# Optimization experiments

Measured on AMD Instinct MI355X. Metric: run time of the kernel, lower is better.

The kernel has to match this reference:

```python
import jax, jax.numpy as jnp
import numpy as np

B, T, D = 256, 336, 128
H = 1024
N_LABEL, LABEL_CLASS = 24, 1
FORGET_BIAS = 1.0  # TF BasicLSTMCell default


def setup_inputs() -> dict:
    key = jax.random.key(0)
    ks = jax.random.split(key, 8)
    s1 = 1.0 / np.sqrt(D + H)
    s2 = 1.0 / np.sqrt(2 * H)
    sd = 1.0 / np.sqrt(H)
    return {
        "features": jax.random.normal(ks[0], (B, T, D), jnp.float32),
        "labels": jax.random.normal(ks[1], (B, N_LABEL, LABEL_CLASS), jnp.float32),
        "W1": jax.random.normal(ks[2], (D + H, 4 * H), jnp.float32) * s1,
        "b1": jnp.zeros((4 * H,), jnp.float32),
        "W2": jax.random.normal(ks[3], (2 * H, 4 * H), jnp.float32) * s2,
        "b2": jnp.zeros((4 * H,), jnp.float32),
        "Wd": jax.random.normal(ks[4], (H, N_LABEL * LABEL_CLASS), jnp.float32) * sd,
        "bd": jnp.zeros((N_LABEL * LABEL_CLASS,), jnp.float32),
    }


def _lstm_cell(c, h, x, W, b):
    # TF BasicLSTMCell: gates = [x, h] @ W + b, split into i, j, f, o
    z = jnp.concatenate([x, h], axis=-1) @ W + b
    i, j, f, o = jnp.split(z, 4, axis=-1)
    new_c = c * jax.nn.sigmoid(f + FORGET_BIAS) + jax.nn.sigmoid(i) * jnp.tanh(j)
    new_h = jnp.tanh(new_c) * jax.nn.sigmoid(o)
    return new_c, new_h


def reference(features, labels, W1, b1, W2, b2, Wd, bd):
    batch = features.shape[0]
    zeros = jnp.zeros((batch, H), features.dtype)
    init = (zeros, zeros, zeros, zeros)  # c1, h1, c2, h2

    def step(carry, x_t):
        c1, h1, c2, h2 = carry
        c1, h1 = _lstm_cell(c1, h1, x_t, W1, b1)
        c2, h2 = _lstm_cell(c2, h2, h1, W2, b2)
        return (c1, h1, c2, h2), None

    xs = jnp.swapaxes(features, 0, 1)  # [T, B, D]
    (c1, h1, c2, h2), _ = jax.lax.scan(step, init, xs)
    # dense head on last-timestep output of top layer
    pred = (h2 @ Wd + bd).reshape(batch, N_LABEL, LABEL_CLASS)
    loss = jnp.mean(jnp.square(pred - labels))
    return loss
```

## Files before the change

### kernel.cpp

```cpp
#include <hip/hip_runtime.h>

#define TT 336
#define BB 256
#define DD 128
#define HH 1024
#define TD 43008
#define BBHH 262144

#define SSU0 20480u
#define SSU1 32768u
#define LBU1 5242880u

typedef __attribute__((ext_vector_type(8))) short short8;
typedef __attribute__((ext_vector_type(8))) unsigned short ushort8;
typedef __attribute__((ext_vector_type(4))) unsigned short ushort4v;
typedef __attribute__((ext_vector_type(4))) float floatx4;

#define OFF_ZPAD 0u
#define OFF_C1   4096u
#define OFF_C2   1052672u
#define OFF_H1   2101248u
#define OFF_H2   3149824u
#define OFF_B1P  4198400u
#define OFF_B2P  4214784u
#define OFF_X    4231168u
#define OFF_BP   26251264u

static __device__ __forceinline__ unsigned short f2bf(float f) {
  unsigned int x = __float_as_uint(f);
  x += 0x7fffu + ((x >> 16) & 1u);
  return (unsigned short)(x >> 16);
}
static __device__ __forceinline__ float bf2f(unsigned short u) {
  return __uint_as_float(((unsigned int)u) << 16);
}
static __device__ __forceinline__ float sigm(float x) {
  return 1.f / (1.f + __expf(-x));
}
static __device__ __forceinline__ float tanh_fast(float x) {
  float ax = fabsf(x);
  float e = __expf(-2.f * ax);
  float t = (1.f - e) / (1.f + e);
  return x < 0.f ? -t : t;
}

#define GLOAD_LDS16(gsrc, ldst)                                              \
  __builtin_amdgcn_global_load_lds(                                          \
      (const __attribute__((address_space(1))) void*)(gsrc),                 \
      (__attribute__((address_space(3))) void*)(ldst), 16, 0, 0)

__global__ __launch_bounds__(256) void init_zero(float* out, uint4* span, long n16) {
  long i = (long)blockIdx.x * 256 + threadIdx.x;
  if (i < n16) span[i] = make_uint4(0u, 0u, 0u, 0u);
  if (i == 0) out[0] = 0.f;
}

__global__ __launch_bounds__(256) void feat2bf(const float* __restrict__ in,
                                               unsigned short* __restrict__ out, long nq) {
  long Q = (long)blockIdx.x * 256 + threadIdx.x;
  if (Q >= nq) return;
  int b = (int)(Q / 5376);
  long outQ = (Q & ~7L) | ((Q ^ (long)b) & 7);
  const floatx4* pp = (const floatx4*)(in + Q * 8);
  floatx4 a = pp[0], c = pp[1];
  ushort8 v;
  #pragma unroll
  for (int q = 0; q < 4; ++q) { v[q] = f2bf(a[q]); v[4 + q] = f2bf(c[q]); }
  *(ushort8*)(out + outQ * 8) = v;
}

__global__ __launch_bounds__(256) void bpack(const float* __restrict__ W1,
                                             const float* __restrict__ W2,
                                             unsigned short* __restrict__ out) {
  __shared__ unsigned short tile[64][72];
  int bid = blockIdx.x, t = threadIdx.x;
  int L, tk, tn;
  if (bid < 1280) { L = 0; tk = bid % 20; tn = bid / 20; }
  else            { L = 1; tk = (bid - 1280) % 32; tn = (bid - 1280) / 32; }
  const float* W = L ? W2 : W1;
  int KG = L ? 512 : 320;
  int k0 = tk * 64, n0p = tn * 64;
  int g = k0 / KG;
  int ksg0 = (k0 - g * KG) >> 5;
  int ntile = n0p >> 7, wn = (n0p >> 6) & 1;
  unsigned int SSu = L ? SSU1 : SSU0;
  unsigned int base = (L ? LBU1 : 0u) + ntile * 8u * SSu + (g * 2 + wn) * SSu;

  #pragma unroll
  for (int i = 0; i < 16; ++i) {
    int idx = i * 256 + t;
    int kk = idx >> 6, nn = idx & 63;
    int np = n0p + nn;
    int norig = ((np & 3) << 10) + (np >> 2);
    float v = 0.f;
    if (!(L == 0 && k0 + kk >= 1152)) v = W[(size_t)(k0 + kk) * 4096 + norig];
    tile[kk][nn] = f2bf(v);
  }
  __syncthreads();
  int t64 = t & 63;
  #pragma unroll
  for (int pass = 0; pass < 2; ++pass) {
    int f = (t >> 6) + pass * 4;
    int ksl = f >> 2, ni = f & 3;
    ushort8 v;
    #pragma unroll
    for (int j = 0; j < 8; ++j)
      v[j] = tile[ksl * 32 + ((t64 >> 4) << 3) + j][ni * 16 + (t64 & 15)];
    *(ushort8*)(out + base + (unsigned)((ksg0 + ksl) * 4 + ni) * 512u + t64 * 8) = v;
  }
}

__global__ __launch_bounds__(256) void bias_perm(const float* __restrict__ b1,
                                                 const float* __restrict__ b2,
                                                 float* __restrict__ b1p,
                                                 float* __restrict__ b2p) {
  int idx = blockIdx.x * 256 + threadIdx.x;
  const float* src = (idx < 4096) ? b1 : b2;
  float* dst = (idx < 4096) ? b1p : b2p;
  int n = idx & 4095;
  dst[n] = src[(n & 3) * 1024 + (n >> 2)];
}

__global__ __launch_bounds__(512, 2) void gemm_cell(
    const unsigned short* __restrict__ Xbf,
    unsigned short* __restrict__ h1bufs, unsigned short* __restrict__ h2bufs,
    const unsigned short* __restrict__ Bpack,
    const float* __restrict__ b1p, const float* __restrict__ b2p,
    float* __restrict__ c1, float* __restrict__ c2,
    const unsigned short* __restrict__ zpad,
    int p, int do1, int do2) {
  __shared__ __align__(16) unsigned short Abuf[4][2][64 * 64];
  __shared__ __align__(16) float zt0[64 * 132];
  __shared__ __align__(16) float zt1[64 * 132];

  int bid = blockIdx.x;
  int layer = bid >> 7;
  if (layer == 0 ? !do1 : !do2) return;
  int lid = bid & 127;
  int ntile = (lid & 7) | (((lid >> 5) & 3) << 3);
  int mtile = (lid >> 3) & 3;
  int m0 = mtile * 64;
  int u0 = ntile * 32;

  const unsigned short* hp1 = h1bufs + (size_t)(p & 1) * BBHH;
  const unsigned short* hp2 = h2bufs + (size_t)(p & 1) * BBHH;
  const int KG = layer ? 512 : 320;
  const int NIT = KG >> 6;

  int tid = threadIdx.x;
  int g = tid >> 7;
  int wn = (tid >> 6) & 1;
  int lane = tid & 63;
  int kgbase = g * KG;

  unsigned int SSu = layer ? SSU1 : SSU0;
  const unsigned short* bwave =
      Bpack + (layer ? LBU1 : 0u) + ntile * 8u * SSu + (unsigned)(g * 2 + wn) * SSu;

  auto stageA = [&](int buf, int it) {
    int kb = kgbase + (it << 6);
    unsigned short* dst0 = &Abuf[g][buf][0];
    #pragma unroll
    for (int c = 0; c < 4; ++c) {
      int rowbase = c * 16 + wn * 8;
      int rg = m0 + rowbase + (lane >> 3);
      int kq = lane & 7;
      const unsigned short* src;
      if (layer == 0) {
        if (kb < DD)        src = Xbf + (size_t)rg * TD + p * DD + kb + kq * 8;
        else if (kb < 1152) src = hp1 + (size_t)rg * HH + (kb - DD) + kq * 8;
        else                src = zpad + lane * 8;
      } else {
        if (kb < HH) src = hp1 + (size_t)rg * HH + kb + kq * 8;
        else         src = hp2 + (size_t)rg * HH + (kb - HH) + kq * 8;
      }
      GLOAD_LDS16(src, dst0 + rowbase * 64);
    }
  };
  auto loadB = [&](ushort8 (&dst)[2][4], int it) {
    #pragma unroll
    for (int ksl = 0; ksl < 2; ++ksl)
      #pragma unroll
      for (int ni = 0; ni < 4; ++ni)
        dst[ksl][ni] =
            *(const ushort8*)(bwave + (unsigned)((it * 2 + ksl) * 4 + ni) * 512u + lane * 8);
  };

  floatx4 acc[4][4];
  #pragma unroll
  for (int i = 0; i < 4; ++i)
    #pragma unroll
    for (int j = 0; j < 4; ++j) acc[i][j] = (floatx4){0.f, 0.f, 0.f, 0.f};

  ushort8 bc[2][4], bn[2][4];
  stageA(0, 0);
  loadB(bc, 0);

  for (int it = 0; it < NIT; ++it) {
    int buf = it & 1;
    __syncthreads();
    if (it + 1 < NIT) { stageA(buf ^ 1, it + 1); loadB(bn, it + 1); }
    const unsigned short* Ab = &Abuf[g][buf][0];
    #pragma unroll
    for (int ksl = 0; ksl < 2; ++ksl) {
      int qb = ksl * 4 + (lane >> 4);
      short8 af[4];
      #pragma unroll
      for (int mi = 0; mi < 4; ++mi) {
        int ml = mi * 16 + (lane & 15);
        af[mi] = *(const short8*)&Ab[ml * 64 + ((qb ^ (ml & 7)) << 3)];
      }
      #pragma unroll
      for (int mi = 0; mi < 4; ++mi)
        #pragma unroll
        for (int ni = 0; ni < 4; ++ni)
          acc[mi][ni] = __builtin_amdgcn_mfma_f32_16x16x32_bf16(
              af[mi], (short8)bc[ksl][ni], acc[mi][ni], 0, 0, 0);
    }
    #pragma unroll
    for (int ksl = 0; ksl < 2; ++ksl)
      #pragma unroll
      for (int ni = 0; ni < 4; ++ni) bc[ksl][ni] = bn[ksl][ni];
  }

  float* ztw = (g & 1) ? zt1 : zt0;
  if (g < 2) {
    #pragma unroll
    for (int mi = 0; mi < 4; ++mi)
      #pragma unroll
      for (int ni = 0; ni < 4; ++ni)
        #pragma unroll
        for (int rr = 0; rr < 4; ++rr) {
          int row = mi * 16 + (lane >> 4) * 4 + rr;
          int col = wn * 64 + ni * 16 + (lane & 15);
          ztw[row * 132 + col] = acc[mi][ni][rr];
        }
  }
  __syncthreads();
  if (g >= 2) {
    #pragma unroll
    for (int mi = 0; mi < 4; ++mi)
      #pragma unroll
      for (int ni = 0; ni < 4; ++ni)
        #pragma unroll
        for (int rr = 0; rr < 4; ++rr) {
          int row = mi * 16 + (lane >> 4) * 4 + rr;
          int col = wn * 64 + ni * 16 + (lane & 15);
          ztw[row * 132 + col] += acc[mi][ni][rr];
        }
  }
  __syncthreads();

  {
    unsigned short* hn = (layer ? h2bufs : h1bufs) + (size_t)((p + 1) & 1) * BBHH;
    int r = tid >> 3, ug = tid & 7;
    int rg = m0 + r;
    float* cp = (layer ? c2 : c1) + (size_t)rg * HH + u0 + ug * 4;
    const float* bp = (layer ? b2p : b1p) + (size_t)(u0 + ug * 4) * 4;
    floatx4 cold = *(const floatx4*)cp;
    floatx4 cn;
    ushort4v hv;
    #pragma unroll
    for (int k = 0; k < 4; ++k) {
      int cbase = r * 132 + (ug * 4 + k) * 4;
      floatx4 gt0 = *(const floatx4*)&zt0[cbase];
      floatx4 gt1 = *(const floatx4*)&zt1[cbase];
      floatx4 bb = *(const floatx4*)&bp[k * 4];
      float i_ = gt0[0] + gt1[0] + bb[0];
      float j_ = gt0[1] + gt1[1] + bb[1];
      float f_ = gt0[2] + gt1[2] + bb[2] + 1.f;
      float o_ = gt0[3] + gt1[3] + bb[3];
      float nc = cold[k] * sigm(f_) + sigm(i_) * tanh_fast(j_);
      cn[k] = nc;
      hv[k] = f2bf(tanh_fast(nc) * sigm(o_));
    }
    *(floatx4*)cp = cn;
    int q = (u0 >> 3) + (ug >> 1);
    *(ushort4v*)&hn[(size_t)rg * HH + (((q & ~7) | ((q ^ rg) & 7)) << 3) + (ug & 1) * 4] = hv;
  }
}

__global__ __launch_bounds__(64) void head_loss(const unsigned short* __restrict__ h2,
                                                const float* __restrict__ Wd,
                                                const float* __restrict__ bd,
                                                const float* __restrict__ labels,
                                                float* __restrict__ out) {
  int b = blockIdx.x;
  int l = threadIdx.x;
  float pacc[24];
  #pragma unroll
  for (int n = 0; n < 24; ++n) pacc[n] = 0.f;
  for (int k = l; k < HH; k += 64) {
    int ksw = (k & ~63) | ((((k >> 3) ^ b) & 7) << 3) | (k & 7);
    float hv = bf2f(h2[(size_t)b * HH + ksw]);
    const float* wr = Wd + (size_t)k * 24;
    #pragma unroll
    for (int n = 0; n < 24; ++n) pacc[n] += hv * wr[n];
  }
  #pragma unroll
  for (int n = 0; n < 24; ++n) {
    float v = pacc[n];
    for (int off = 32; off > 0; off >>= 1) v += __shfl_down(v, off);
    pacc[n] = v;
  }
  if (l == 0) {
    float s = 0.f;
    #pragma unroll
    for (int n = 0; n < 24; ++n) {
      float pred = pacc[n] + bd[n];
      float d = pred - labels[b * 24 + n];
      s += d * d;
    }
    atomicAdd(out, s * (1.0f / 6144.0f));
  }
}

extern "C" void kernel_launch(void* const* d_in, const int* in_sizes, int n_in,
                              void* d_out, int out_size, void* d_ws, size_t ws_size,
                              hipStream_t stream) {
  const float* features = (const float*)d_in[0];
  const float* labels   = (const float*)d_in[1];
  const float* W1 = (const float*)d_in[2];
  const float* b1 = (const float*)d_in[3];
  const float* W2 = (const float*)d_in[4];
  const float* b2 = (const float*)d_in[5];
  const float* Wd = (const float*)d_in[6];
  const float* bd = (const float*)d_in[7];

  char* ws = (char*)d_ws;
  unsigned short* zpad = (unsigned short*)(ws + OFF_ZPAD);
  float*          c1   = (float*)(ws + OFF_C1);
  float*          c2   = (float*)(ws + OFF_C2);
  unsigned short* h1   = (unsigned short*)(ws + OFF_H1);
  unsigned short* h2   = (unsigned short*)(ws + OFF_H2);
  float*          b1p  = (float*)(ws + OFF_B1P);
  float*          b2p  = (float*)(ws + OFF_B2P);
  unsigned short* Xbf  = (unsigned short*)(ws + OFF_X);
  unsigned short* BP   = (unsigned short*)(ws + OFF_BP);
  float* out = (float*)d_out;

  init_zero<<<1026, 256, 0, stream>>>(out, (uint4*)ws, 262400L);
  feat2bf<<<5376, 256, 0, stream>>>(features, Xbf, 1376256L);
  bpack<<<3328, 256, 0, stream>>>(W1, W2, BP);
  bias_perm<<<32, 256, 0, stream>>>(b1, b2, b1p, b2p);

  for (int p = 0; p <= TT; ++p) {
    gemm_cell<<<256, 512, 0, stream>>>(Xbf, h1, h2, BP, b1p, b2p, c1, c2, zpad,
                                       p, p < TT ? 1 : 0, p >= 1 ? 1 : 0);
  }
  head_loss<<<256, 64, 0, stream>>>(h2 + BBHH, Wd, bd, labels, out);
}
```

Measured before the change: 6.519 ms.

## Replace per-timestep launches with persistent LSTM kernel and grid barrier

Merges the 337 per-timestep gemm_cell launches into a single persistent kernel that loops over timesteps and uses an atomic-counter grid barrier between steps. Cell state and biases now stay in registers instead of being reloaded and stored in global memory every step. h-buffer loads use a cache-policy flag (aux=17) so freshly written data from other blocks is read coherently. This removes launch overhead and per-step c traffic, but needs all 256 blocks to be co-resident and adds spin-wait barrier latency.

```diff
diff --git a/kernel.cpp b/kernel.cpp
--- a/kernel.cpp
+++ b/kernel.cpp
@@ -17,8 +17,7 @@
 typedef __attribute__((ext_vector_type(4))) float floatx4;
 
 #define OFF_ZPAD 0u
-#define OFF_C1   4096u
-#define OFF_C2   1052672u
+#define OFF_BAR  4096u
 #define OFF_H1   2101248u
 #define OFF_H2   3149824u
 #define OFF_B1P  4198400u
@@ -48,6 +47,10 @@
   __builtin_amdgcn_global_load_lds(                                          \
       (const __attribute__((address_space(1))) void*)(gsrc),                 \
       (__attribute__((address_space(3))) void*)(ldst), 16, 0, 0)
+#define GLOAD_LDS16_DC(gsrc, ldst)                                           \
+  __builtin_amdgcn_global_load_lds(                                          \
+      (const __attribute__((address_space(1))) void*)(gsrc),                 \
+      (__attribute__((address_space(3))) void*)(ldst), 16, 0, 17)
 
 __global__ __launch_bounds__(256) void init_zero(float* out, uint4* span, long n16) {
   long i = (long)blockIdx.x * 256 + threadIdx.x;
@@ -121,29 +124,24 @@
   dst[n] = src[(n & 3) * 1024 + (n >> 2)];
 }
 
-__global__ __launch_bounds__(512, 2) void gemm_cell(
+__global__ __launch_bounds__(512, 2) void lstm_persist(
     const unsigned short* __restrict__ Xbf,
     unsigned short* __restrict__ h1bufs, unsigned short* __restrict__ h2bufs,
     const unsigned short* __restrict__ Bpack,
     const float* __restrict__ b1p, const float* __restrict__ b2p,
-    float* __restrict__ c1, float* __restrict__ c2,
     const unsigned short* __restrict__ zpad,
-    int p, int do1, int do2) {
+    unsigned int* __restrict__ bar) {
   __shared__ __align__(16) unsigned short Abuf[4][2][64 * 64];
   __shared__ __align__(16) float zt0[64 * 132];
   __shared__ __align__(16) float zt1[64 * 132];
 
   int bid = blockIdx.x;
   int layer = bid >> 7;
-  if (layer == 0 ? !do1 : !do2) return;
   int lid = bid & 127;
   int ntile = (lid & 7) | (((lid >> 5) & 3) << 3);
   int mtile = (lid >> 3) & 3;
   int m0 = mtile * 64;
   int u0 = ntile * 32;
-
-  const unsigned short* hp1 = h1bufs + (size_t)(p & 1) * BBHH;
-  const unsigned short* hp2 = h2bufs + (size_t)(p & 1) * BBHH;
   const int KG = layer ? 512 : 320;
   const int NIT = KG >> 6;
 
@@ -157,126 +155,155 @@
   const unsigned short* bwave =
       Bpack + (layer ? LBU1 : 0u) + ntile * 8u * SSu + (unsigned)(g * 2 + wn) * SSu;
 
-  auto stageA = [&](int buf, int it) {
-    int kb = kgbase + (it << 6);
-    unsigned short* dst0 = &Abuf[g][buf][0];
-    #pragma unroll
-    for (int c = 0; c < 4; ++c) {
-      int rowbase = c * 16 + wn * 8;
-      int rg = m0 + rowbase + (lane >> 3);
-      int kq = lane & 7;
-      const unsigned short* src;
-      if (layer == 0) {
-        if (kb < DD)        src = Xbf + (size_t)rg * TD + p * DD + kb + kq * 8;
-        else if (kb < 1152) src = hp1 + (size_t)rg * HH + (kb - DD) + kq * 8;
-        else                src = zpad + lane * 8;
-      } else {
-        if (kb < HH) src = hp1 + (size_t)rg * HH + kb + kq * 8;
-        else         src = hp2 + (size_t)rg * HH + (kb - HH) + kq * 8;
+  int r = tid >> 3, ug = tid & 7;
+  int rgc = m0 + r;
+  const float* bp = (layer ? b2p : b1p) + (size_t)(u0 + ug * 4) * 4;
+  floatx4 breg[4];
+  #pragma unroll
+  for (int k = 0; k < 4; ++k) breg[k] = *(const floatx4*)&bp[k * 4];
+  floatx4 creg = (floatx4){0.f, 0.f, 0.f, 0.f};
+
+  for (int p = 0; p <= TT; ++p) {
+    bool active = layer ? (p >= 1) : (p < TT);
+    if (active) {
+      const unsigned short* hp1 = h1bufs + (size_t)(p & 1) * BBHH;
+      const unsigned short* hp2 = h2bufs + (size_t)(p & 1) * BBHH;
+
+      auto stageA = [&](int buf, int it) {
+        int kb = kgbase + (it << 6);
+        unsigned short* dst0 = &Abuf[g][buf][0];
+        #pragma unroll
+        for (int c = 0; c < 4; ++c) {
+          int rowbase = c * 16 + wn * 8;
+          int rg = m0 + rowbase + (lane >> 3);
+          int kq = lane & 7;
+          if (layer == 0) {
+            if (kb < DD) {
+              GLOAD_LDS16(Xbf + (size_t)rg * TD + p * DD + kb + kq * 8,
+                          dst0 + rowbase * 64);
+            } else if (kb < 1152) {
+              GLOAD_LDS16_DC(hp1 + (size_t)rg * HH + (kb - DD) + kq * 8,
+                             dst0 + rowbase * 64);
+            } else {
+              GLOAD_LDS16(zpad + lane * 8, dst0 + rowbase * 64);
+            }
+          } else {
+            if (kb < HH) {
+              GLOAD_LDS16_DC(hp1 + (size_t)rg * HH + kb + kq * 8,
+                             dst0 + rowbase * 64);
+            } else {
+              GLOAD_LDS16_DC(hp2 + (size_t)rg * HH + (kb - HH) + kq * 8,
+                             dst0 + rowbase * 64);
+            }
+          }
+        }
+      };
+      auto loadB = [&](ushort8 (&dst)[2][4], int it) {
+        #pragma unroll
+        for (int ksl = 0; ksl < 2; ++ksl)
+          #pragma unroll
+          for (int ni = 0; ni < 4; ++ni)
+            dst[ksl][ni] =
+                *(const ushort8*)(bwave + (unsigned)((it * 2 + ksl) * 4 + ni) * 512u + lane * 8);
+      };
+
+      floatx4 acc[4][4];
+      #pragma unroll
+      for (int i = 0; i < 4; ++i)
+        #pragma unroll
+        for (int j = 0; j < 4; ++j) acc[i][j] = (floatx4){0.f, 0.f, 0.f, 0.f};
+
+      ushort8 bc[2][4], bn[2][4];
+      stageA(0, 0);
+      loadB(bc, 0);
+
+      for (int it = 0; it < NIT; ++it) {
+        int buf = it & 1;
+        __syncthreads();
+        if (it + 1 < NIT) { stageA(buf ^ 1, it + 1); loadB(bn, it + 1); }
+        const unsigned short* Ab = &Abuf[g][buf][0];
+        #pragma unroll
+        for (int ksl = 0; ksl < 2; ++ksl) {
+          int qb = ksl * 4 + (lane >> 4);
+          short8 af[4];
+          #pragma unroll
+          for (int mi = 0; mi < 4; ++mi) {
+            int ml = mi * 16 + (lane & 15);
+            af[mi] = *(const short8*)&Ab[ml * 64 + ((qb ^ (ml & 7)) << 3)];
+          }
+          #pragma unroll
+          for (int mi = 0; mi < 4; ++mi)
+            #pragma unroll
+            for (int ni = 0; ni < 4; ++ni)
+              acc[mi][ni] = __builtin_amdgcn_mfma_f32_16x16x32_bf16(
+                  af[mi], (short8)bc[ksl][ni], acc[mi][ni], 0, 0, 0);
+        }
+        #pragma unroll
+        for (int ksl = 0; ksl < 2; ++ksl)
+          #pragma unroll
+          for (int ni = 0; ni < 4; ++ni) bc[ksl][ni] = bn[ksl][ni];
       }
-      GLOAD_LDS16(src, dst0 + rowbase * 64);
+
+      float* ztw = (g & 1) ? zt1 : zt0;
+      if (g < 2) {
+        #pragma unroll
+        for (int mi = 0; mi < 4; ++mi)
+          #pragma unroll
+          for (int ni = 0; ni < 4; ++ni)
+            #pragma unroll
+            for (int rr = 0; rr < 4; ++rr) {
+              int row = mi * 16 + (lane >> 4) * 4 + rr;
+              int col = wn * 64 + ni * 16 + (lane & 15);
+              ztw[row * 132 + col] = acc[mi][ni][rr];
+            }
+      }
+      __syncthreads();
+      if (g >= 2) {
+        #pragma unroll
+        for (int mi = 0; mi < 4; ++mi)
+          #pragma unroll
+          for (int ni = 0; ni < 4; ++ni)
+            #pragma unroll
+            for (int rr = 0; rr < 4; ++rr) {
+              int row = mi * 16 + (lane >> 4) * 4 + rr;
+              int col = wn * 64 + ni * 16 + (lane & 15);
+              ztw[row * 132 + col] += acc[mi][ni][rr];
+            }
+      }
+      __syncthreads();
+
+      {
+        unsigned short* hn = (layer ? h2bufs : h1bufs) + (size_t)((p + 1) & 1) * BBHH;
+        floatx4 cold = creg, cn;
+        ushort4v hv;
+        #pragma unroll
+        for (int k = 0; k < 4; ++k) {
+          int cbase = r * 132 + (ug * 4 + k) * 4;
+          floatx4 gt0 = *(const floatx4*)&zt0[cbase];
+          floatx4 gt1 = *(const floatx4*)&zt1[cbase];
+          floatx4 bb = breg[k];
+          float i_ = gt0[0] + gt1[0] + bb[0];
+          float j_ = gt0[1] + gt1[1] + bb[1];
+          float f_ = gt0[2] + gt1[2] + bb[2] + 1.f;
+          float o_ = gt0[3] + gt1[3] + bb[3];
+          float nc = cold[k] * sigm(f_) + sigm(i_) * tanh_fast(j_);
+          cn[k] = nc;
+          hv[k] = f2bf(tanh_fast(nc) * sigm(o_));
+        }
+        creg = cn;
+        int q = (u0 >> 3) + (ug >> 1);
+        *(ushort4v*)&hn[(size_t)rgc * HH + (((q & ~7) | ((q ^ rgc) & 7)) << 3) + (ug & 1) * 4] = hv;
+      }
     }
-  };
-  auto loadB = [&](ushort8 (&dst)[2][4], int it) {
-    #pragma unroll
-    for (int ksl = 0; ksl < 2; ++ksl)
-      #pragma unroll
-      for (int ni = 0; ni < 4; ++ni)
-        dst[ksl][ni] =
-            *(const ushort8*)(bwave + (unsigned)((it * 2 + ksl) * 4 + ni) * 512u + lane * 8);
-  };
-
-  floatx4 acc[4][4];
-  #pragma unroll
-  for (int i = 0; i < 4; ++i)
-    #pragma unroll
-    for (int j = 0; j < 4; ++j) acc[i][j] = (floatx4){0.f, 0.f, 0.f, 0.f};
-
-  ushort8 bc[2][4], bn[2][4];
-  stageA(0, 0);
-  loadB(bc, 0);
-
-  for (int it = 0; it < NIT; ++it) {
-    int buf = it & 1;
+
     __syncthreads();
-    if (it + 1 < NIT) { stageA(buf ^ 1, it + 1); loadB(bn, it + 1); }
-    const unsigned short* Ab = &Abuf[g][buf][0];
-    #pragma unroll
-    for (int ksl = 0; ksl < 2; ++ksl) {
-      int qb = ksl * 4 + (lane >> 4);
-      short8 af[4];
-      #pragma unroll
-      for (int mi = 0; mi < 4; ++mi) {
-        int ml = mi * 16 + (lane & 15);
-        af[mi] = *(const short8*)&Ab[ml * 64 + ((qb ^ (ml & 7)) << 3)];
-      }
-      #pragma unroll
-      for (int mi = 0; mi < 4; ++mi)
-        #pragma unroll
-        for (int ni = 0; ni < 4; ++ni)
-          acc[mi][ni] = __builtin_amdgcn_mfma_f32_16x16x32_bf16(
-              af[mi], (short8)bc[ksl][ni], acc[mi][ni], 0, 0, 0);
+    if (tid == 0) {
+      __hip_atomic_fetch_add(bar, 1u, __ATOMIC_RELEASE, __HIP_MEMORY_SCOPE_AGENT);
+      unsigned int want = 256u * (unsigned int)(p + 1);
+      while (__hip_atomic_load(bar, __ATOMIC_RELAXED, __HIP_MEMORY_SCOPE_AGENT) < want)
+        __builtin_amdgcn_s_sleep(1);
     }
-    #pragma unroll
-    for (int ksl = 0; ksl < 2; ++ksl)
-      #pragma unroll
-      for (int ni = 0; ni < 4; ++ni) bc[ksl][ni] = bn[ksl][ni];
-  }
-
-  float* ztw = (g & 1) ? zt1 : zt0;
-  if (g < 2) {
-    #pragma unroll
-    for (int mi = 0; mi < 4; ++mi)
-      #pragma unroll
-      for (int ni = 0; ni < 4; ++ni)
-        #pragma unroll
-        for (int rr = 0; rr < 4; ++rr) {
-          int row = mi * 16 + (lane >> 4) * 4 + rr;
-          int col = wn * 64 + ni * 16 + (lane & 15);
-          ztw[row * 132 + col] = acc[mi][ni][rr];
-        }
-  }
-  __syncthreads();
-  if (g >= 2) {
-    #pragma unroll
-    for (int mi = 0; mi < 4; ++mi)
-      #pragma unroll
-      for (int ni = 0; ni < 4; ++ni)
-        #pragma unroll
-        for (int rr = 0; rr < 4; ++rr) {
-          int row = mi * 16 + (lane >> 4) * 4 + rr;
-          int col = wn * 64 + ni * 16 + (lane & 15);
-          ztw[row * 132 + col] += acc[mi][ni][rr];
-        }
-  }
-  __syncthreads();
-
-  {
-    unsigned short* hn = (layer ? h2bufs : h1bufs) + (size_t)((p + 1) & 1) * BBHH;
-    int r = tid >> 3, ug = tid & 7;
-    int rg = m0 + r;
-    float* cp = (layer ? c2 : c1) + (size_t)rg * HH + u0 + ug * 4;
-    const float* bp = (layer ? b2p : b1p) + (size_t)(u0 + ug * 4) * 4;
-    floatx4 cold = *(const floatx4*)cp;
-    floatx4 cn;
-    ushort4v hv;
-    #pragma unroll
-    for (int k = 0; k < 4; ++k) {
-      int cbase = r * 132 + (ug * 4 + k) * 4;
-      floatx4 gt0 = *(const floatx4*)&zt0[cbase];
-      floatx4 gt1 = *(const floatx4*)&zt1[cbase];
-      floatx4 bb = *(const floatx4*)&bp[k * 4];
-      float i_ = gt0[0] + gt1[0] + bb[0];
-      float j_ = gt0[1] + gt1[1] + bb[1];
-      float f_ = gt0[2] + gt1[2] + bb[2] + 1.f;
-      float o_ = gt0[3] + gt1[3] + bb[3];
-      float nc = cold[k] * sigm(f_) + sigm(i_) * tanh_fast(j_);
-      cn[k] = nc;
-      hv[k] = f2bf(tanh_fast(nc) * sigm(o_));
-    }
-    *(floatx4*)cp = cn;
-    int q = (u0 >> 3) + (ug >> 1);
-    *(ushort4v*)&hn[(size_t)rg * HH + (((q & ~7) | ((q ^ rg) & 7)) << 3) + (ug & 1) * 4] = hv;
+    __syncthreads();
   }
 }
 
@@ -329,8 +356,7 @@
 
   char* ws = (char*)d_ws;
   unsigned short* zpad = (unsigned short*)(ws + OFF_ZPAD);
-  float*          c1   = (float*)(ws + OFF_C1);
-  float*          c2   = (float*)(ws + OFF_C2);
+  unsigned int*   bar  = (unsigned int*)(ws + OFF_BAR);
   unsigned short* h1   = (unsigned short*)(ws + OFF_H1);
   unsigned short* h2   = (unsigned short*)(ws + OFF_H2);
   float*          b1p  = (float*)(ws + OFF_B1P);
@@ -344,9 +370,7 @@
   bpack<<<3328, 256, 0, stream>>>(W1, W2, BP);
   bias_perm<<<32, 256, 0, stream>>>(b1, b2, b1p, b2p);
 
-  for (int p = 0; p <= TT; ++p) {
-    gemm_cell<<<256, 512, 0, stream>>>(Xbf, h1, h2, BP, b1p, b2p, c1, c2, zpad,
-                                       p, p < TT ? 1 : 0, p >= 1 ? 1 : 0);
-  }
+  lstm_persist<<<256, 512, 0, stream>>>(Xbf, h1, h2, BP, b1p, b2p, zpad, bar);
+
   head_loss<<<256, 64, 0, stream>>>(h2 + BBHH, Wd, bd, labels, out);
 }
```

New measurement: 10.41 ms. 1.6x slower.
